# Kernel optimization log

Measured on AMD Instinct MI355X. Metric: run time of the kernel, lower is better.

Reference implementation:

```python
import jax, jax.numpy as jnp
import numpy as np

H = 16
NEG = -1e10

def setup_inputs() -> dict:
    key = jax.random.key(0)
    ks = jax.random.split(key, 12)
    B, S, D = 2, 2048, 1024
    sc = 1.0 / np.sqrt(D)
    inp = {
        'q': jax.random.normal(ks[0], (B, S, D), jnp.float32),
        'k': jax.random.normal(ks[1], (B, S, D), jnp.float32),
        'v': jax.random.normal(ks[2], (B, S, D), jnp.float32),
        'Wq': jax.random.normal(ks[3], (D, D), jnp.float32) * sc,
        'bq': jax.random.normal(ks[4], (D,), jnp.float32) * 0.02,
        'Wk': jax.random.normal(ks[5], (D, D), jnp.float32) * sc,
        'bk': jax.random.normal(ks[6], (D,), jnp.float32) * 0.02,
        'Wv': jax.random.normal(ks[7], (D, D), jnp.float32) * sc,
        'bv': jax.random.normal(ks[8], (D,), jnp.float32) * 0.02,
        'Wo': jax.random.normal(ks[9], (D, D), jnp.float32) * sc,
        'bo': jax.random.normal(ks[10], (D,), jnp.float32) * 0.02,
        'mask': jax.random.randint(ks[11], (B, S, S), 0, 2, jnp.int32),
    }
    return inp

def reference(q, k, v, Wq, bq, Wk, bk, Wv, bv, Wo, bo, mask):
    B, S, D = q.shape
    dk = D // H
    # projections (torch Linear: x @ W.T + b), split heads -> [B,H,S,dk]
    qh = (q @ Wq.T + bq).reshape(B, S, H, dk).transpose(0, 2, 1, 3)
    kh = (k @ Wk.T + bk).reshape(B, S, H, dk).transpose(0, 2, 1, 3)
    vh = (v @ Wv.T + bv).reshape(B, S, H, dk).transpose(0, 2, 1, 3)
    # scaled dot-product scores [B,H,Sq,Sk]
    scores = jnp.einsum('bhqd,bhkd->bhqk', qh, kh) / jnp.sqrt(jnp.float32(dk))
    scores = jnp.where(mask[:, None, :, :] == 0, jnp.float32(NEG), scores)
    attn = jax.nn.softmax(scores, axis=-1)  # dropout in eval mode = identity
    ctx = jnp.einsum('bhqk,bhkd->bhqd', attn, vh)
    concat = ctx.transpose(0, 2, 1, 3).reshape(B, S, D)
    return concat @ Wo.T + bo
```

## Files before the change

### kernel.cpp

```cpp
#include <hip/hip_runtime.h>
#include <hip/hip_bf16.h>
#include <stdint.h>

typedef __bf16 bf16;
typedef __bf16 bf16x2 __attribute__((ext_vector_type(2)));
typedef __bf16 bf16x4 __attribute__((ext_vector_type(4)));
typedef __bf16 bf16x8 __attribute__((ext_vector_type(8)));
typedef float f32x4 __attribute__((ext_vector_type(4)));
typedef float f32x16 __attribute__((ext_vector_type(16)));
typedef unsigned int u32;
typedef u32 u32x4 __attribute__((ext_vector_type(4)));
typedef unsigned long long u64;

#define MFMA16(a, b, c) __builtin_amdgcn_mfma_f32_16x16x32_bf16((a), (b), (c), 0, 0, 0)
#define MFMA32(a, b, c) __builtin_amdgcn_mfma_f32_32x32x16_bf16((a), (b), (c), 0, 0, 0)

constexpr int Bc = 2, Sc = 2048, Dc = 1024, Hc = 16, DKc = 64;
constexpr int Mc = Bc * Sc;
constexpr int MW = Sc / 64;
#define QSCALE 0.1803368801111731f

__device__ __forceinline__ u32 pk2(float a, float b) {
  bf16x2 t; t[0] = (bf16)a; t[1] = (bf16)b;
  return __builtin_bit_cast(u32, t);
}

__device__ __forceinline__ void gl_lds16(const void* g, void* l) {
  __builtin_amdgcn_global_load_lds((const __attribute__((address_space(1))) void*)g,
                                   (__attribute__((address_space(3))) void*)l, 16, 0, 0);
}

__global__ __launch_bounds__(256) void prep_kernel(
    const float* __restrict__ wq, const float* __restrict__ wk,
    const float* __restrict__ wv, const float* __restrict__ wo,
    const float* __restrict__ q, const float* __restrict__ k, const float* __restrict__ v,
    const int* __restrict__ mask,
    bf16* __restrict__ dwq, bf16* __restrict__ dwk, bf16* __restrict__ dwv,
    bf16* __restrict__ dwo, bf16* __restrict__ dq, bf16* __restrict__ dk,
    bf16* __restrict__ dv, u64* __restrict__ mbT) {
  const int y = blockIdx.y;
  if (y == 7) {
    const int lane = threadIdx.x & 63;
    const int wid = (blockIdx.x * blockDim.x + threadIdx.x) >> 6;
    const int nw = (gridDim.x * blockDim.x) >> 6;
    const int nwords = Bc * Sc * Sc / 64;
    for (int i = wid; i < nwords; i += nw) {
      int vv = mask[(size_t)i * 64 + lane];
      u64 bits = __ballot(vv != 0);
      if (lane == 0) {
        const int kw = i & (MW - 1), bq = i >> 5;
        const int b = bq >> 11, qq = bq & (Sc - 1);
        mbT[((size_t)(b * MW + kw)) * Sc + qq] = bits;
      }
    }
    return;
  }
  const float* src; bf16* dst; size_t n;
  switch (y) {
    case 0: src = wq; dst = dwq; n = (size_t)Dc * Dc; break;
    case 1: src = wk; dst = dwk; n = (size_t)Dc * Dc; break;
    case 2: src = wv; dst = dwv; n = (size_t)Dc * Dc; break;
    case 3: src = wo; dst = dwo; n = (size_t)Dc * Dc; break;
    case 4: src = q;  dst = dq;  n = (size_t)Mc * Dc; break;
    case 5: src = k;  dst = dk;  n = (size_t)Mc * Dc; break;
    default: src = v; dst = dv;  n = (size_t)Mc * Dc; break;
  }
  const size_t i = ((size_t)blockIdx.x * 256 + threadIdx.x) * 8;
  if (i >= n) return;
  const float sc = (y == 0) ? QSCALE : 1.0f;
  f32x4 x0 = *(const f32x4*)&src[i];
  f32x4 x1 = *(const f32x4*)&src[i + 4];
  bf16x8 o;
#pragma unroll
  for (int j = 0; j < 4; ++j) { o[j] = (bf16)(x0[j] * sc); o[4 + j] = (bf16)(x1[j] * sc); }
  *(bf16x8*)&dst[i] = o;
}

__global__ __launch_bounds__(256, 3) void gemm_qkv_kernel(
    const bf16* __restrict__ qb, const bf16* __restrict__ kb, const bf16* __restrict__ vb,
    const bf16* __restrict__ wq, const bf16* __restrict__ wk, const bf16* __restrict__ wv,
    const float* __restrict__ bq, const float* __restrict__ bk, const float* __restrict__ bv,
    bf16* __restrict__ qh, bf16* __restrict__ kh, bf16* __restrict__ vt) {
  __shared__ bf16 As[128 * 64];
  __shared__ bf16 Bs[128 * 64];
  const int d = blockIdx.x;
  const int xcd = d & 7, idx = d >> 3;
  const int proj = idx >> 5, w = idx & 31;
  const int n0 = (w & 7) * 128;
  const int m0 = (xcd * 4 + (w >> 3)) * 128;
  const bf16* Af = proj == 0 ? qb : proj == 1 ? kb : vb;
  const bf16* Bw = proj == 0 ? wq : proj == 1 ? wk : wv;
  const float* bias = proj == 0 ? bq : proj == 1 ? bk : bv;

  const int t = threadIdx.x, lane = t & 63, wv4 = t >> 6;
  const int c = lane & 15, g = lane >> 4;
  const int wr = wv4 >> 1, wc = wv4 & 1;

  f32x4 acc[4][4];
#pragma unroll
  for (int i = 0; i < 4; ++i)
#pragma unroll
    for (int j = 0; j < 4; ++j) acc[i][j] = (f32x4){0.f, 0.f, 0.f, 0.f};

  const int brow_l = lane >> 3;
  const int bslot_l = (lane & 7) ^ brow_l;

  for (int k0 = 0; k0 < Dc; k0 += 64) {
#pragma unroll
    for (int u = 0; u < 4; ++u) {
      const int ch = wv4 * 4 + u;
      const int row = ch * 8 + brow_l;
      gl_lds16(&Af[(size_t)(m0 + row) * Dc + k0 + bslot_l * 8], &As[ch * 512]);
    }
#pragma unroll
    for (int u = 0; u < 4; ++u) {
      const int ch = wv4 * 4 + u;
      const int row = ch * 8 + brow_l;
      gl_lds16(&Bw[(size_t)(n0 + row) * Dc + k0 + bslot_l * 8], &Bs[ch * 512]);
    }
    __syncthreads();
#pragma unroll
    for (int ks = 0; ks < 2; ++ks) {
      bf16x8 af[4], bfr[4];
#pragma unroll
      for (int mt = 0; mt < 4; ++mt) {
        const int row = wr * 64 + mt * 16 + c;
        const int sl = (4 * ks + g) ^ (c & 7);
        af[mt] = *(const bf16x8*)&As[row * 64 + sl * 8];
      }
#pragma unroll
      for (int nt = 0; nt < 4; ++nt) {
        const int row = wc * 64 + nt * 16 + c;
        const int sl = (4 * ks + g) ^ (c & 7);
        bfr[nt] = *(const bf16x8*)&Bs[row * 64 + sl * 8];
      }
#pragma unroll
      for (int mt = 0; mt < 4; ++mt)
#pragma unroll
        for (int nt = 0; nt < 4; ++nt) acc[mt][nt] = MFMA16(af[mt], bfr[nt], acc[mt][nt]);
    }
    __syncthreads();
  }

  const float bsc = proj == 0 ? QSCALE : 1.0f;
  const int colb = n0 + wc * 64 + c;
  const int mrowb = m0 + wr * 64 + 4 * g;
#pragma unroll
  for (int mt = 0; mt < 4; ++mt) {
#pragma unroll
    for (int nt = 0; nt < 4; ++nt) {
      const int col = colb + nt * 16;
      const int mrow = mrowb + mt * 16;
      const float bb = bias[col] * bsc;
      f32x4 a = acc[mt][nt];
      if (proj == 0) {
#pragma unroll
        for (int r = 0; r < 4; ++r) qh[(size_t)(mrow + r) * Dc + col] = (bf16)(a[r] + bb);
      } else if (proj == 1) {
        const int hh = col >> 6, dd = col & 63;
#pragma unroll
        for (int r = 0; r < 4; ++r) {
          const int mr = mrow + r;
          kh[((size_t)((mr >> 11) * Hc + hh) * Sc + (mr & (Sc - 1))) * DKc + dd] = (bf16)(a[r] + bb);
        }
      } else {
        const int batch = mrow >> 11, s = mrow & (Sc - 1);
        const int s2 = (s & ~15) | ((s & 4) << 1) | ((s & 8) >> 1);
        const int hh = col >> 6, dd = col & 63;
        bf16x4 pkv;
#pragma unroll
        for (int r = 0; r < 4; ++r) pkv[r] = (bf16)(a[r] + bb);
        *(bf16x4*)&vt[((size_t)((batch * Hc + hh) * DKc + dd)) * Sc + s2] = pkv;
      }
    }
  }
}

__global__ __launch_bounds__(256, 2) void gemm_o_kernel(const bf16* __restrict__ ctxp,
                                                        const bf16* __restrict__ wo,
                                                        const float* __restrict__ bo,
                                                        float* __restrict__ outp) {
  __shared__ bf16 As[128 * 64];
  __shared__ bf16 Bs[64 * 64];
  const int d = blockIdx.x;
  const int xcd = d & 7, idx = d >> 3;
  const int n0 = (idx & 15) * 64;
  const int m0 = (xcd * 4 + (idx >> 4)) * 128;

  const int t = threadIdx.x, lane = t & 63, wv4 = t >> 6;
  const int c = lane & 15, g = lane >> 4;
  const int brow_l = lane >> 3;
  const int bslot_l = (lane & 7) ^ brow_l;

  f32x4 acc[2][4];
#pragma unroll
  for (int i = 0; i < 2; ++i)
#pragma unroll
    for (int j = 0; j < 4; ++j) acc[i][j] = (f32x4){0.f, 0.f, 0.f, 0.f};

  for (int k0 = 0; k0 < Dc; k0 += 64) {
#pragma unroll
    for (int u = 0; u < 4; ++u) {
      const int ch = wv4 * 4 + u;
      const int row = ch * 8 + brow_l;
      gl_lds16(&ctxp[(size_t)(m0 + row) * Dc + k0 + bslot_l * 8], &As[ch * 512]);
    }
    {
      const int ch = wv4;
      const int row = ch * 8 + brow_l;
      gl_lds16(&wo[(size_t)(n0 + row) * Dc + k0 + bslot_l * 8], &Bs[ch * 512]);
      const int ch2 = 4 + wv4;
      const int row2 = ch2 * 8 + brow_l;
      gl_lds16(&wo[(size_t)(n0 + row2) * Dc + k0 + bslot_l * 8], &Bs[ch2 * 512]);
    }
    __syncthreads();
#pragma unroll
    for (int ks = 0; ks < 2; ++ks) {
      bf16x8 af[2], bfr[4];
#pragma unroll
      for (int mt = 0; mt < 2; ++mt) {
        const int row = wv4 * 32 + mt * 16 + c;
        const int sl = (4 * ks + g) ^ (c & 7);
        af[mt] = *(const bf16x8*)&As[row * 64 + sl * 8];
      }
#pragma unroll
      for (int nt = 0; nt < 4; ++nt) {
        const int row = nt * 16 + c;
        const int sl = (4 * ks + g) ^ (c & 7);
        bfr[nt] = *(const bf16x8*)&Bs[row * 64 + sl * 8];
      }
#pragma unroll
      for (int mt = 0; mt < 2; ++mt)
#pragma unroll
        for (int nt = 0; nt < 4; ++nt) acc[mt][nt] = MFMA16(af[mt], bfr[nt], acc[mt][nt]);
    }
    __syncthreads();
  }

  const int colb = n0 + c;
  const int mrowb = m0 + wv4 * 32 + 4 * g;
#pragma unroll
  for (int mt = 0; mt < 2; ++mt)
#pragma unroll
    for (int nt = 0; nt < 4; ++nt) {
      const int col = colb + nt * 16;
      const int mrow = mrowb + mt * 16;
      const float bb = bo[col];
      f32x4 a = acc[mt][nt];
#pragma unroll
      for (int r = 0; r < 4; ++r) outp[(size_t)(mrow + r) * Dc + col] = a[r] + bb;
    }
}

template <int SPLITS>
__global__ __launch_bounds__(512, 4) void attn_kernel(const bf16* __restrict__ qh,
                                                      const bf16* __restrict__ kh,
                                                      const bf16* __restrict__ vt,
                                                      const u64* __restrict__ mbT,
                                                      bf16* __restrict__ ctx,
                                                      float* __restrict__ opart,
                                                      float* __restrict__ lsums) {
  __shared__ bf16 Ks[2][64 * 64];
  __shared__ bf16 Vs[2][64 * 64];
  const int d = blockIdx.x;
  const int xcd = d & 7, idx = d >> 3;
  const int bh = xcd * 4 + idx / (8 * SPLITS);
  const int sub = idx % (8 * SPLITS);
  const int qt = sub / SPLITS, half = sub % SPLITS;
  const int b = bh >> 4, h = bh & 15;
  const int lane = threadIdx.x & 63, wv8 = threadIdx.x >> 6;
  const int ql = lane & 31, hi = lane >> 5;
  const int qrow = qt * 256 + wv8 * 32 + ql;

  const bf16* Qp = qh + (size_t)(b * Sc + qrow) * Dc + h * DKc;
  const bf16* Kp = kh + (size_t)(b * Hc + h) * Sc * DKc;
  const bf16* Vp = vt + (size_t)(b * Hc + h) * DKc * Sc;
  const u64* mbp = mbT + (size_t)b * MW * Sc;

  const int k0 = half * (Sc / SPLITS);
  constexpr int NIT = (Sc / SPLITS) / 64;

  const int srow = lane >> 3, sslot = lane & 7;
  auto stage = [&](int buf, int kt) {
    const int r = wv8 * 8 + srow;
    gl_lds16(&Kp[(size_t)(kt + r) * DKc + (size_t)((sslot ^ srow) * 8)], &Ks[buf][wv8 * 512]);
    gl_lds16(&Vp[(size_t)r * Sc + kt + (size_t)((sslot ^ srow) * 8)], &Vs[buf][wv8 * 512]);
  };

  bf16x8 qf[4];
#pragma unroll
  for (int ka = 0; ka < 4; ++ka) qf[ka] = *(const bf16x8*)&Qp[16 * ka + 8 * hi];

  bf16x8 ones8;
#pragma unroll
  for (int j = 0; j < 8; ++j) ones8[j] = (bf16)1.0f;

  f32x16 oacc[2], lacc;
#pragma unroll
  for (int i = 0; i < 2; ++i)
#pragma unroll
    for (int r = 0; r < 16; ++r) oacc[i][r] = 0.f;
#pragma unroll
  for (int r = 0; r < 16; ++r) lacc[r] = 0.f;

  stage(0, k0);
  u64 w = mbp[(size_t)(k0 >> 6) * Sc + qrow];
  asm volatile("s_waitcnt vmcnt(0)" ::: "memory");
  __builtin_amdgcn_s_barrier();
  __builtin_amdgcn_sched_barrier(0);

  for (int it = 0; it < NIT; ++it) {
    const int kt = k0 + it * 64;
    const int buf = it & 1;
    const int ktn = (it + 1 < NIT) ? kt + 64 : kt;
    stage(buf ^ 1, ktn);
    const u64 wn = mbp[(size_t)(ktn >> 6) * Sc + qrow];

    f32x16 st[2];
#pragma unroll
    for (int tt = 0; tt < 2; ++tt) {
      const int row = 32 * tt + ql;
      const bf16* kbase = &Ks[buf][row * 64];
      f32x16 z;
#pragma unroll
      for (int r = 0; r < 16; ++r) z[r] = 0.f;
      __builtin_amdgcn_s_setprio(1);
#pragma unroll
      for (int ka = 0; ka < 4; ++ka) {
        bf16x8 kf = *(const bf16x8*)&kbase[((2 * ka + hi) ^ (row & 7)) * 8];
        z = MFMA32(kf, qf[ka], z);
      }
      __builtin_amdgcn_s_setprio(0);
      st[tt] = z;
    }

    const u32 wt0 = (u32)(w >> (4 * hi));
    const u32 wt1 = (u32)(w >> (32 + 4 * hi));
#pragma unroll
    for (int tt = 0; tt < 2; ++tt) {
      const u32 wt = tt ? wt1 : wt0;
#pragma unroll
      for (int r = 0; r < 16; ++r) {
        const int bit = (r & 3) + 8 * (r >> 2);
        const float p = __builtin_amdgcn_exp2f((float)st[tt][r]);
        st[tt][r] = ((wt >> bit) & 1u) ? p : 0.f;
      }
    }

    u32x4 pb[4];
#pragma unroll
    for (int ks = 0; ks < 4; ++ks) {
      const int tt = ks >> 1, e = ks & 1;
#pragma unroll
      for (int w2 = 0; w2 < 4; ++w2)
        pb[ks][w2] = pk2((float)st[tt][8 * e + 2 * w2], (float)st[tt][8 * e + 2 * w2 + 1]);
    }

    __builtin_amdgcn_s_setprio(1);
#pragma unroll
    for (int ks = 0; ks < 4; ++ks)
      lacc = MFMA32(ones8, __builtin_bit_cast(bf16x8, pb[ks]), lacc);
#pragma unroll
    for (int dt = 0; dt < 2; ++dt) {
      const int row = 32 * dt + ql;
      const bf16* vbase = &Vs[buf][row * 64];
#pragma unroll
      for (int ks = 0; ks < 4; ++ks) {
        bf16x8 vf = *(const bf16x8*)&vbase[((2 * ks + hi) ^ (row & 7)) * 8];
        oacc[dt] = MFMA32(vf, __builtin_bit_cast(bf16x8, pb[ks]), oacc[dt]);
      }
    }
    __builtin_amdgcn_s_setprio(0);

    asm volatile("s_waitcnt vmcnt(0)" ::: "memory");
    __builtin_amdgcn_s_barrier();
    __builtin_amdgcn_sched_barrier(0);
    w = wn;
  }

  const float lsum = lacc[0];
  if constexpr (SPLITS > 1) {
    float* opr = opart + ((size_t)(half * 32 + bh) * Sc + qrow) * 64;
#pragma unroll
    for (int dt = 0; dt < 2; ++dt)
#pragma unroll
      for (int i = 0; i < 4; ++i) {
        f32x4 o4;
#pragma unroll
        for (int rr = 0; rr < 4; ++rr) o4[rr] = oacc[dt][4 * i + rr];
        *(f32x4*)&opr[32 * dt + 8 * i + 4 * hi] = o4;
      }
    if (hi == 0) lsums[(size_t)(half * 32 + bh) * Sc + qrow] = lsum;
  } else {
    const float rinv = 1.f / fmaxf(lsum, 1e-35f);
    bf16* cp = ctx + (size_t)(b * Sc + qrow) * Dc + h * DKc;
#pragma unroll
    for (int dt = 0; dt < 2; ++dt)
#pragma unroll
      for (int i = 0; i < 4; ++i) {
        bf16x4 o4;
#pragma unroll
        for (int rr = 0; rr < 4; ++rr) o4[rr] = (bf16)(oacc[dt][4 * i + rr] * rinv);
        *(bf16x4*)&cp[32 * dt + 8 * i + 4 * hi] = o4;
      }
  }
}

template <int NS>
__global__ __launch_bounds__(256) void combine_kernel(const float* __restrict__ op,
                                                      const float* __restrict__ ls,
                                                      bf16* __restrict__ ctx) {
  const int wv = threadIdx.x >> 6, lane = threadIdx.x & 63;
  const size_t row = (size_t)blockIdx.x * 4 + wv;
  const int bh = (int)(row >> 11), q = (int)(row & 2047);
  const int b = bh >> 4, h = bh & 15;
  float o = 0.f, l = 0.f;
#pragma unroll
  for (int s = 0; s < NS; ++s) {
    o += op[(size_t)s * 65536 * 64 + row * 64 + lane];
    l += ls[(size_t)s * 65536 + row];
  }
  ctx[((size_t)(b * Sc + q)) * Dc + h * DKc + lane] = (bf16)(o / fmaxf(l, 1e-35f));
}

extern "C" void kernel_launch(void* const* d_in, const int* in_sizes, int n_in,
                              void* d_out, int out_size, void* d_ws, size_t ws_size,
                              hipStream_t stream) {
  (void)in_sizes; (void)n_in; (void)out_size;
  const float* q  = (const float*)d_in[0];
  const float* k  = (const float*)d_in[1];
  const float* v  = (const float*)d_in[2];
  const float* Wq = (const float*)d_in[3];
  const float* bq = (const float*)d_in[4];
  const float* Wk = (const float*)d_in[5];
  const float* bk = (const float*)d_in[6];
  const float* Wv = (const float*)d_in[7];
  const float* bv = (const float*)d_in[8];
  const float* Wo = (const float*)d_in[9];
  const float* bo = (const float*)d_in[10];
  const int* mask = (const int*)d_in[11];

  char* ws = (char*)d_ws;
  size_t off = 0;
  auto take = [&](size_t bytes) -> void* {
    void* p = ws + off;
    off += (bytes + 255) & ~(size_t)255;
    return p;
  };
  bf16* qh  = (bf16*)take((size_t)Mc * Dc * 2);
  bf16* kh  = (bf16*)take((size_t)Mc * Dc * 2);
  bf16* vt  = (bf16*)take((size_t)Mc * Dc * 2);
  bf16* ctx = (bf16*)take((size_t)Mc * Dc * 2);
  u64* mbits = (u64*)take((size_t)Bc * Sc * MW * 8);
  bf16* wqb = (bf16*)take((size_t)Dc * Dc * 2);
  bf16* wkb = (bf16*)take((size_t)Dc * Dc * 2);
  bf16* wvb = (bf16*)take((size_t)Dc * Dc * 2);
  bf16* wob = (bf16*)take((size_t)Dc * Dc * 2);
  bf16* qb  = (bf16*)take((size_t)Mc * Dc * 2);
  bf16* kb  = (bf16*)take((size_t)Mc * Dc * 2);
  bf16* vb  = (bf16*)take((size_t)Mc * Dc * 2);

  const size_t opart_sz = (size_t)32 * Sc * 64 * 4;
  const size_t ls_sz    = (size_t)32 * Sc * 4;
  int splits = 1;
  float* opart = nullptr; float* lsums = nullptr;
  if (off + (opart_sz + ls_sz) * 2 <= ws_size) {
    splits = 2;
    opart = (float*)(ws + off);
    lsums = (float*)(ws + off + opart_sz * 2);
  }

  prep_kernel<<<dim3(2048, 8), 256, 0, stream>>>(Wq, Wk, Wv, Wo, q, k, v, mask,
                                                 wqb, wkb, wvb, wob, qb, kb, vb, mbits);
  gemm_qkv_kernel<<<768, 256, 0, stream>>>(qb, kb, vb, wqb, wkb, wvb, bq, bk, bv, qh, kh, vt);
  if (splits == 2) {
    attn_kernel<2><<<512, 512, 0, stream>>>(qh, kh, vt, mbits, ctx, opart, lsums);
    combine_kernel<2><<<16384, 256, 0, stream>>>(opart, lsums, ctx);
  } else {
    attn_kernel<1><<<256, 512, 0, stream>>>(qh, kh, vt, mbits, ctx, opart, lsums);
  }
  gemm_o_kernel<<<512, 256, 0, stream>>>(ctx, wob, bo, (float*)d_out);
}
```

Baseline: 155.8 us.

## Fuse split-attention combine into output projection GEMM A-tile load

Removes the separate combine kernel that merged the two attention split partials into a bf16 context buffer. The output-projection GEMM now reads both fp32 partial outputs and lse sums directly, normalizes them, converts to bf16 and writes the swizzled A tile into LDS. This saves a kernel launch plus a full write and read of the context tensor. In exchange the GEMM's A load becomes synchronous register loads of twice as much fp32 data, repeated for each of the 16 column blocks, rather than async global-to-LDS copies.

```diff
diff --git a/kernel.cpp b/kernel.cpp
--- a/kernel.cpp
+++ b/kernel.cpp
@@ -176,7 +176,10 @@
   }
 }
 
+template <int FUSED>
 __global__ __launch_bounds__(256, 2) void gemm_o_kernel(const bf16* __restrict__ ctxp,
+                                                        const float* __restrict__ op,
+                                                        const float* __restrict__ ls,
                                                         const bf16* __restrict__ wo,
                                                         const float* __restrict__ bo,
                                                         float* __restrict__ outp) {
@@ -192,6 +195,9 @@
   const int brow_l = lane >> 3;
   const int bslot_l = (lane & 7) ^ brow_l;
 
+  const int arow = t >> 1;
+  const int acol0 = (t & 1) * 32;
+
   f32x4 acc[2][4];
 #pragma unroll
   for (int i = 0; i < 2; ++i)
@@ -199,11 +205,37 @@
     for (int j = 0; j < 4; ++j) acc[i][j] = (f32x4){0.f, 0.f, 0.f, 0.f};
 
   for (int k0 = 0; k0 < Dc; k0 += 64) {
-#pragma unroll
-    for (int u = 0; u < 4; ++u) {
-      const int ch = wv4 * 4 + u;
-      const int row = ch * 8 + brow_l;
-      gl_lds16(&ctxp[(size_t)(m0 + row) * Dc + k0 + bslot_l * 8], &As[ch * 512]);
+    if constexpr (FUSED) {
+      const int mr = m0 + arow;
+      const int bh = (mr >> 11) * Hc + (k0 >> 6);
+      const int qq = mr & (Sc - 1);
+      const size_t r0 = ((size_t)bh * Sc + qq) * 64;
+      const size_t r1 = ((size_t)(bh + 32) * Sc + qq) * 64;
+      const float l = ls[(size_t)bh * Sc + qq] + ls[(size_t)(bh + 32) * Sc + qq];
+      const float rinv = 1.f / fmaxf(l, 1e-35f);
+#pragma unroll
+      for (int seg = 0; seg < 4; ++seg) {
+        const int cbase = acol0 + seg * 8;
+        f32x4 lo0 = *(const f32x4*)&op[r0 + cbase];
+        f32x4 hi0 = *(const f32x4*)&op[r0 + cbase + 4];
+        f32x4 lo1 = *(const f32x4*)&op[r1 + cbase];
+        f32x4 hi1 = *(const f32x4*)&op[r1 + cbase + 4];
+        bf16x8 o8;
+#pragma unroll
+        for (int j = 0; j < 4; ++j) {
+          o8[j] = (bf16)((lo0[j] + lo1[j]) * rinv);
+          o8[4 + j] = (bf16)((hi0[j] + hi1[j]) * rinv);
+        }
+        const int slot = ((cbase >> 3)) ^ (arow & 7);
+        *(bf16x8*)&As[arow * 64 + slot * 8] = o8;
+      }
+    } else {
+#pragma unroll
+      for (int u = 0; u < 4; ++u) {
+        const int ch = wv4 * 4 + u;
+        const int row = ch * 8 + brow_l;
+        gl_lds16(&ctxp[(size_t)(m0 + row) * Dc + k0 + bslot_l * 8], &As[ch * 512]);
+      }
     }
     {
       const int ch = wv4;
@@ -406,23 +438,6 @@
   }
 }
 
-template <int NS>
-__global__ __launch_bounds__(256) void combine_kernel(const float* __restrict__ op,
-                                                      const float* __restrict__ ls,
-                                                      bf16* __restrict__ ctx) {
-  const int wv = threadIdx.x >> 6, lane = threadIdx.x & 63;
-  const size_t row = (size_t)blockIdx.x * 4 + wv;
-  const int bh = (int)(row >> 11), q = (int)(row & 2047);
-  const int b = bh >> 4, h = bh & 15;
-  float o = 0.f, l = 0.f;
-#pragma unroll
-  for (int s = 0; s < NS; ++s) {
-    o += op[(size_t)s * 65536 * 64 + row * 64 + lane];
-    l += ls[(size_t)s * 65536 + row];
-  }
-  ctx[((size_t)(b * Sc + q)) * Dc + h * DKc + lane] = (bf16)(o / fmaxf(l, 1e-35f));
-}
-
 extern "C" void kernel_launch(void* const* d_in, const int* in_sizes, int n_in,
                               void* d_out, int out_size, void* d_ws, size_t ws_size,
                               hipStream_t stream) {
@@ -475,9 +490,9 @@
   gemm_qkv_kernel<<<768, 256, 0, stream>>>(qb, kb, vb, wqb, wkb, wvb, bq, bk, bv, qh, kh, vt);
   if (splits == 2) {
     attn_kernel<2><<<512, 512, 0, stream>>>(qh, kh, vt, mbits, ctx, opart, lsums);
-    combine_kernel<2><<<16384, 256, 0, stream>>>(opart, lsums, ctx);
+    gemm_o_kernel<1><<<512, 256, 0, stream>>>(ctx, opart, lsums, wob, bo, (float*)d_out);
   } else {
     attn_kernel<1><<<256, 512, 0, stream>>>(qh, kh, vt, mbits, ctx, opart, lsums);
-  }
-  gemm_o_kernel<<<512, 256, 0, stream>>>(ctx, wob, bo, (float*)d_out);
-}
+    gemm_o_kernel<0><<<512, 256, 0, stream>>>(ctx, opart, lsums, wob, bo, (float*)d_out);
+  }
+}
```

Measured after the change: 200.3 us. 1.29x slower.

## Fuse split-attention combine into output projection GEMM

Applied to the files above, without the earlier changes.

Removes the separate combine kernel. The output-projection GEMM now reads the two fp32 partial attention outputs and their row sums directly, normalises them and converts to bf16 while loading the A operand. This drops a kernel launch and the write and re-read of the bf16 context buffer. In exchange, the GEMM loads twice as many fp32 A bytes (two partials) per tile, uses smaller 64-row tiles with 4-way occupancy, and has no double-buffering.

```diff
diff --git a/kernel.cpp b/kernel.cpp
--- a/kernel.cpp
+++ b/kernel.cpp
@@ -176,6 +176,97 @@
   }
 }
 
+__global__ __launch_bounds__(256, 4) void gemm_o_fused_kernel(const float* __restrict__ op,
+                                                              const float* __restrict__ ls,
+                                                              const bf16* __restrict__ wo,
+                                                              const float* __restrict__ bo,
+                                                              float* __restrict__ outp) {
+  __shared__ float Asf[2][64 * 64];
+  __shared__ bf16 Bs[64 * 64];
+  const int d = blockIdx.x;
+  const int xcd = d & 7, idx = d >> 3;
+  const int panel = xcd * 8 + (idx >> 4);
+  const int m0 = panel * 64;
+  const int n0 = (idx & 15) * 64;
+  const int batch = m0 >> 11;
+
+  const int t = threadIdx.x, lane = t & 63, wv = t >> 6;
+  const int c = lane & 15, g = lane >> 4;
+
+  const int arow_l = lane >> 4;
+  const int aslot_l = lane & 15;
+  const int brow_l = lane >> 3;
+  const int bslot_l = (lane & 7) ^ brow_l;
+
+  const int myrow = wv * 16 + c;
+  const int myq = (m0 + myrow) & (Sc - 1);
+
+  f32x4 acc[4];
+#pragma unroll
+  for (int j = 0; j < 4; ++j) acc[j] = (f32x4){0.f, 0.f, 0.f, 0.f};
+
+  for (int k0 = 0; k0 < Dc; k0 += 64) {
+    const int h = k0 >> 6;
+    const int bh = batch * Hc + h;
+    const float l0 = ls[(size_t)bh * Sc + myq];
+    const float l1 = ls[(size_t)(32 + bh) * Sc + myq];
+#pragma unroll
+    for (int hf = 0; hf < 2; ++hf)
+#pragma unroll
+      for (int u = 0; u < 4; ++u) {
+        const int ch = wv * 4 + u;
+        const int row = ch * 4 + arow_l;
+        const int gsrc = aslot_l ^ (row & 7);
+        const size_t src =
+            (((size_t)(hf * 32 + bh)) * Sc + ((m0 + row) & (Sc - 1))) * 64 + gsrc * 4;
+        gl_lds16(&op[src], &Asf[hf][ch * 256]);
+      }
+    {
+      const int row = wv * 8 + brow_l;
+      gl_lds16(&wo[(size_t)(n0 + row) * Dc + k0 + bslot_l * 8], &Bs[wv * 512]);
+      const int row2 = (wv + 4) * 8 + brow_l;
+      gl_lds16(&wo[(size_t)(n0 + row2) * Dc + k0 + bslot_l * 8], &Bs[(wv + 4) * 512]);
+    }
+    __syncthreads();
+
+    const float rinv = 1.f / fmaxf(l0 + l1, 1e-35f);
+#pragma unroll
+    for (int ks = 0; ks < 2; ++ks) {
+      const int s0 = (8 * ks + 2 * g) ^ (myrow & 7);
+      const int s1 = (8 * ks + 2 * g + 1) ^ (myrow & 7);
+      f32x4 a00 = *(const f32x4*)&Asf[0][myrow * 64 + s0 * 4];
+      f32x4 a01 = *(const f32x4*)&Asf[0][myrow * 64 + s1 * 4];
+      f32x4 a10 = *(const f32x4*)&Asf[1][myrow * 64 + s0 * 4];
+      f32x4 a11 = *(const f32x4*)&Asf[1][myrow * 64 + s1 * 4];
+      bf16x8 af;
+#pragma unroll
+      for (int j = 0; j < 4; ++j) {
+        af[j] = (bf16)((a00[j] + a10[j]) * rinv);
+        af[4 + j] = (bf16)((a01[j] + a11[j]) * rinv);
+      }
+#pragma unroll
+      for (int nt = 0; nt < 4; ++nt) {
+        const int row = nt * 16 + c;
+        const int sl = (4 * ks + g) ^ (c & 7);
+        bf16x8 bfr = *(const bf16x8*)&Bs[row * 64 + sl * 8];
+        acc[nt] = MFMA16(af, bfr, acc[nt]);
+      }
+    }
+    __syncthreads();
+  }
+
+  const int colb = n0 + c;
+  const int mrowb = m0 + wv * 16 + 4 * g;
+#pragma unroll
+  for (int nt = 0; nt < 4; ++nt) {
+    const int col = colb + nt * 16;
+    const float bb = bo[col];
+    f32x4 a = acc[nt];
+#pragma unroll
+    for (int r = 0; r < 4; ++r) outp[(size_t)(mrowb + r) * Dc + col] = a[r] + bb;
+  }
+}
+
 __global__ __launch_bounds__(256, 2) void gemm_o_kernel(const bf16* __restrict__ ctxp,
                                                         const bf16* __restrict__ wo,
                                                         const float* __restrict__ bo,
@@ -406,23 +497,6 @@
   }
 }
 
-template <int NS>
-__global__ __launch_bounds__(256) void combine_kernel(const float* __restrict__ op,
-                                                      const float* __restrict__ ls,
-                                                      bf16* __restrict__ ctx) {
-  const int wv = threadIdx.x >> 6, lane = threadIdx.x & 63;
-  const size_t row = (size_t)blockIdx.x * 4 + wv;
-  const int bh = (int)(row >> 11), q = (int)(row & 2047);
-  const int b = bh >> 4, h = bh & 15;
-  float o = 0.f, l = 0.f;
-#pragma unroll
-  for (int s = 0; s < NS; ++s) {
-    o += op[(size_t)s * 65536 * 64 + row * 64 + lane];
-    l += ls[(size_t)s * 65536 + row];
-  }
-  ctx[((size_t)(b * Sc + q)) * Dc + h * DKc + lane] = (bf16)(o / fmaxf(l, 1e-35f));
-}
-
 extern "C" void kernel_launch(void* const* d_in, const int* in_sizes, int n_in,
                               void* d_out, int out_size, void* d_ws, size_t ws_size,
                               hipStream_t stream) {
@@ -475,9 +549,9 @@
   gemm_qkv_kernel<<<768, 256, 0, stream>>>(qb, kb, vb, wqb, wkb, wvb, bq, bk, bv, qh, kh, vt);
   if (splits == 2) {
     attn_kernel<2><<<512, 512, 0, stream>>>(qh, kh, vt, mbits, ctx, opart, lsums);
-    combine_kernel<2><<<16384, 256, 0, stream>>>(opart, lsums, ctx);
+    gemm_o_fused_kernel<<<1024, 256, 0, stream>>>(opart, lsums, wob, bo, (float*)d_out);
   } else {
     attn_kernel<1><<<256, 512, 0, stream>>>(qh, kh, vt, mbits, ctx, opart, lsums);
-  }
-  gemm_o_kernel<<<512, 256, 0, stream>>>(ctx, wob, bo, (float*)d_out);
-}
+    gemm_o_kernel<<<512, 256, 0, stream>>>(ctx, wob, bo, (float*)d_out);
+  }
+}
```

Result: slower. 160.2 us (+2.8%).
